# Optimization experiments

Measured on AMD Instinct MI355X. Metric: run time of the kernel, lower is better.

## Reference

```python
import jax, jax.numpy as jnp
import numpy as np
import math

B, T, C = 2, 2048, 1024
H, DK, DV = 16, 64, 64


def setup_inputs() -> dict:
    key = jax.random.key(0)
    ks = jax.random.split(key, 5)
    # randw(*d) = randn(*d) / sqrt(d[-1])
    x = jax.random.normal(ks[0], (B, T, C), dtype=jnp.float32)
    w_q = jax.random.normal(ks[1], (H, DK, C), dtype=jnp.float32) / math.sqrt(C)
    w_k = jax.random.normal(ks[2], (H, DK, C), dtype=jnp.float32) / math.sqrt(C)
    w_v = jax.random.normal(ks[3], (H, DV, C), dtype=jnp.float32) / math.sqrt(C)
    w_o = jax.random.normal(ks[4], (H * DV, C), dtype=jnp.float32) / math.sqrt(C)
    return {"x": x, "w_q": w_q, "w_k": w_k, "w_v": w_v, "w_o": w_o}


def reference(x, w_q, w_k, w_v, w_o):
    # Full prefill: bs_q.first = 0, bs_q.nb = T, causal=True, dropout=0 (eval).
    dk = w_q.shape[1]
    q = jnp.einsum('ntc,hdc->nhtd', x, w_q)  # [B,H,T,DK]
    k = jnp.einsum('ntc,hdc->nhtd', x, w_k)  # [B,H,T,DK]
    v = jnp.einsum('ntc,hdc->nhtd', x, w_v)  # [B,H,T,DV]
    a = jnp.einsum('nhtd,nhsd->nhts', q, k) / jnp.sqrt(jnp.asarray(dk, x.dtype))
    # amm_generator: mask where query_idx < key_idx (strict upper triangle)
    t = a.shape[-1]
    mask = jnp.arange(t)[:, None] < jnp.arange(t)[None, :]  # [T,T] bool
    a = jnp.where(mask[None, None], jnp.asarray(-jnp.inf, a.dtype), a)
    a = jax.nn.softmax(a, axis=-1)
    y = jnp.einsum('nhts,nhsd->nthd', a, v)  # [B,T,H,DV]
    y = y.reshape(y.shape[0], y.shape[1], -1)  # [B,T,H*DV]
    return y @ w_o  # [B,T,C]
```

## Files before the change

kernel.cpp:

```cpp
#include <hip/hip_runtime.h>
#include <hip/hip_bf16.h>

#define B_ 2
#define T_ 2048
#define C_ 1024
#define H_ 16
#define D_ 64

typedef __attribute__((ext_vector_type(8))) short bf16x8;
typedef __attribute__((ext_vector_type(4))) float f32x4;
typedef __attribute__((ext_vector_type(8))) unsigned short u16x8;
typedef __attribute__((ext_vector_type(2))) unsigned int u32x2;
typedef __attribute__((ext_vector_type(4))) unsigned int u32x4;

__device__ __forceinline__ unsigned short bf1(float a) {
    __bf16 x = (__bf16)a;
    return __builtin_bit_cast(unsigned short, x);
}
__device__ __forceinline__ unsigned int pk2(float a, float b) {
    return (unsigned int)bf1(a) | ((unsigned int)bf1(b) << 16);
}

__device__ __forceinline__ void gll16(const void* g, void* l) {
    __builtin_amdgcn_global_load_lds(
        (const __attribute__((address_space(1))) unsigned int*)g,
        (__attribute__((address_space(3))) unsigned int*)l, 16, 0, 0);
}

__global__ __launch_bounds__(256) void prep_x(
    const float* __restrict__ x, unsigned short* __restrict__ xb)
{
    const size_t i = ((size_t)blockIdx.x * 256 + threadIdx.x) * 16;
    float4 f0 = *reinterpret_cast<const float4*>(x + i);
    float4 f1 = *reinterpret_cast<const float4*>(x + i + 4);
    float4 f2 = *reinterpret_cast<const float4*>(x + i + 8);
    float4 f3 = *reinterpret_cast<const float4*>(x + i + 12);
    u32x4 a = {pk2(f0.x, f0.y), pk2(f0.z, f0.w), pk2(f1.x, f1.y), pk2(f1.z, f1.w)};
    u32x4 b = {pk2(f2.x, f2.y), pk2(f2.z, f2.w), pk2(f3.x, f3.y), pk2(f3.z, f3.w)};
    *reinterpret_cast<u32x4*>(xb + i) = a;
    *reinterpret_cast<u32x4*>(xb + i + 8) = b;
}

__global__ __launch_bounds__(256) void prep_w(
    const float* __restrict__ wq, const float* __restrict__ wk,
    const float* __restrict__ wv, unsigned short* __restrict__ wb)
{
    const int bid = blockIdx.x, tid = threadIdx.x;
    const int rb = bid * 4;
    const float* src = (rb < 1024) ? wq + (size_t)rb * 1024
                     : (rb < 2048) ? wk + (size_t)(rb - 1024) * 1024
                                   : wv + (size_t)(rb - 2048) * 1024;
    const float sc = (rb < 1024) ? 0.125f * 1.4426950408889634f : 1.0f;
    const float4* s4 = (const float4*)src;
    u32x2* d = (u32x2*)(wb + (size_t)rb * 1024);
#pragma unroll
    for (int k = 0; k < 4; k++) {
        float4 v = s4[k * 256 + tid];
        u32x2 w;
        w[0] = pk2(v.x * sc, v.y * sc);
        w[1] = pk2(v.z * sc, v.w * sc);
        d[k * 256 + tid] = w;
    }
}

__global__ __launch_bounds__(256) void prep_wo(
    const float* __restrict__ wo, unsigned short* __restrict__ wt)
{
    __shared__ unsigned short tile[64][72];
    const int tk = (blockIdx.x & 15) << 6, tn = (blockIdx.x >> 4) << 6;
    const int r = threadIdx.x >> 2, cb = (threadIdx.x & 3) << 4;
#pragma unroll
    for (int j = 0; j < 4; j++) {
        float4 v = *reinterpret_cast<const float4*>(
            wo + (size_t)(tk + r) * 1024 + tn + cb + j * 4);
        u32x2 w;
        w[0] = pk2(v.x, v.y);
        w[1] = pk2(v.z, v.w);
        *reinterpret_cast<u32x2*>(&tile[r][cb + j * 4]) = w;
    }
    __syncthreads();
    unsigned short buf[16];
#pragma unroll
    for (int j = 0; j < 16; j++) buf[j] = tile[cb + j][r];
    unsigned short* dst = wt + (size_t)(tn + r) * 1024 + tk + cb;
    *reinterpret_cast<u16x8*>(dst) = *reinterpret_cast<u16x8*>(buf);
    *reinterpret_cast<u16x8*>(dst + 8) = *reinterpret_cast<u16x8*>(buf + 8);
}

__global__ __launch_bounds__(256) void qkv_gemm(
    const unsigned short* __restrict__ xb, const unsigned short* __restrict__ wb,
    unsigned short* __restrict__ qkv)
{
    __shared__ __align__(16) unsigned short As[2][128 * 64];
    __shared__ __align__(16) unsigned short Bs[2][128 * 64];
    const int tid = threadIdx.x;
    const int lane = tid & 63, wave = tid >> 6;
    const int g = lane >> 4, c16 = lane & 15;
    const int xcd = blockIdx.x & 7, idx = blockIdx.x >> 3;
    const int bm = (xcd << 2) + idx / 24, bn = idx % 24;
    const int jbase = bn << 7;
    const int which = jbase >> 10;

    const int srow = wave * 32 + (lane >> 3);
    const int swc = ((lane & 7) ^ (lane >> 3)) << 3;
    const unsigned short* asrc = xb + ((size_t)(bm << 7) + srow) * C_ + swc;
    const unsigned short* bsrc = wb + ((size_t)(bn << 7) + srow) * C_ + swc;

    f32x4 acc[4][4];
#pragma unroll
    for (int i = 0; i < 4; i++)
#pragma unroll
        for (int j = 0; j < 4; j++) acc[i][j] = (f32x4){0.f, 0.f, 0.f, 0.f};

    const int wm = (wave >> 1) << 6, wn = (wave & 1) << 6;

    auto stage = [&](int buf, int k0) {
#pragma unroll
        for (int i = 0; i < 4; i++) {
            gll16(asrc + k0 + i * 8 * C_, &As[buf][(wave * 32 + i * 8) << 6]);
            gll16(bsrc + k0 + i * 8 * C_, &Bs[buf][(wave * 32 + i * 8) << 6]);
        }
    };

    stage(0, 0);
    int cur = 0;
    for (int t = 0; t < 16; ++t) {
        __syncthreads();
        if (t < 15) stage(cur ^ 1, (t + 1) << 6);
#pragma unroll
        for (int kk = 0; kk < 2; kk++) {
            bf16x8 af[4], bfv[4];
#pragma unroll
            for (int m = 0; m < 4; m++)
                af[m] = *reinterpret_cast<const bf16x8*>(
                    &As[cur][((wm + m * 16 + c16) << 6) + ((((kk << 2) + g) ^ (c16 & 7)) << 3)]);
#pragma unroll
            for (int n = 0; n < 4; n++)
                bfv[n] = *reinterpret_cast<const bf16x8*>(
                    &Bs[cur][((wn + n * 16 + c16) << 6) + ((((kk << 2) + g) ^ (c16 & 7)) << 3)]);
#pragma unroll
            for (int m = 0; m < 4; m++)
#pragma unroll
                for (int n = 0; n < 4; n++)
                    acc[m][n] = __builtin_amdgcn_mfma_f32_16x16x32_bf16(af[m], bfv[n], acc[m][n], 0, 0, 0);
        }
        cur ^= 1;
    }

#pragma unroll
    for (int m = 0; m < 4; m++) {
        const int grow = (bm << 7) + wm + m * 16 + (g << 2);
#pragma unroll
        for (int n = 0; n < 4; n++) {
            const int j = jbase + wn + n * 16 + c16;
            const int jj = j & 1023;
            const int h = jj >> 6, d = jj & 63;
#pragma unroll
            for (int r = 0; r < 4; r++) {
                const int row = grow + r;
                const int b = row >> 11, t = row & 2047;
                const size_t off = ((size_t)((which * B_ + b) * H_ + h) * T_ + t) * 64 + d;
                qkv[off] = bf1(acc[m][n][r]);
            }
        }
    }
}

__device__ __forceinline__ void attn_tile(
    const unsigned short* __restrict__ Ks, const unsigned short* __restrict__ Vt,
    unsigned short* __restrict__ Psw,
    const bf16x8& qf0, const bf16x8& qf1,
    float& m_run, float& l_run, f32x4* acc,
    int qglob, int s0, bool diag, int g, int c16)
{
    f32x4 sfT[4];
#pragma unroll
    for (int f = 0; f < 4; f++) sfT[f] = (f32x4){0.f, 0.f, 0.f, 0.f};

    __builtin_amdgcn_s_setprio(1);
#pragma unroll
    for (int f = 0; f < 4; f++) {
        const int row = f * 16 + c16;
        const int sw = row & 7;
        bf16x8 k0 = *reinterpret_cast<const bf16x8*>(&Ks[(row << 6) + ((g ^ sw) << 3)]);
        bf16x8 k1 = *reinterpret_cast<const bf16x8*>(&Ks[(row << 6) + (((g + 4) ^ sw) << 3)]);
        sfT[f] = __builtin_amdgcn_mfma_f32_16x16x32_bf16(k0, qf0, sfT[f], 0, 0, 0);
        sfT[f] = __builtin_amdgcn_mfma_f32_16x16x32_bf16(k1, qf1, sfT[f], 0, 0, 0);
    }
    __builtin_amdgcn_s_setprio(0);

    if (diag) {
#pragma unroll
        for (int f = 0; f < 4; f++)
#pragma unroll
            for (int r = 0; r < 4; r++) {
                const int kv = s0 + f * 16 + g * 4 + r;
                if (kv > qglob) sfT[f][r] = -1e30f;
            }
    }

    float mloc = -1e30f;
#pragma unroll
    for (int f = 0; f < 4; f++)
#pragma unroll
        for (int r = 0; r < 4; r++) mloc = fmaxf(mloc, sfT[f][r]);
    mloc = fmaxf(mloc, __shfl_xor(mloc, 16, 64));
    mloc = fmaxf(mloc, __shfl_xor(mloc, 32, 64));
    const float mn = fmaxf(m_run, mloc);
    const float corr = __builtin_amdgcn_exp2f(m_run - mn);
    m_run = mn;
    float ssum = 0.f;
#pragma unroll
    for (int f = 0; f < 4; f++)
#pragma unroll
        for (int r = 0; r < 4; r++) {
            const float pv = __builtin_amdgcn_exp2f(sfT[f][r] - mn);
            sfT[f][r] = pv;
            ssum += pv;
        }
    ssum += __shfl_xor(ssum, 16, 64);
    ssum += __shfl_xor(ssum, 32, 64);
    l_run = l_run * corr + ssum;
#pragma unroll
    for (int fd = 0; fd < 4; fd++)
#pragma unroll
        for (int r = 0; r < 4; r++) acc[fd][r] *= corr;

#pragma unroll
    for (int f = 0; f < 4; f++) {
        u32x2 w;
        w[0] = pk2(sfT[f][0], sfT[f][1]);
        w[1] = pk2(sfT[f][2], sfT[f][3]);
        *reinterpret_cast<u32x2*>(&Psw[c16 * 72 + f * 16 + g * 4]) = w;
    }

    __builtin_amdgcn_s_setprio(1);
#pragma unroll
    for (int ks = 0; ks < 2; ks++) {
        bf16x8 pa = *reinterpret_cast<const bf16x8*>(&Psw[c16 * 72 + ks * 32 + (g << 3)]);
#pragma unroll
        for (int fd = 0; fd < 4; fd++) {
            const int d = fd * 16 + c16;
            bf16x8 vf = *reinterpret_cast<const bf16x8*>(
                &Vt[d * 72 + ((((ks << 2) + g) ^ ((d >> 3) & 7)) << 3)]);
            acc[fd] = __builtin_amdgcn_mfma_f32_16x16x32_bf16(vf, pa, acc[fd], 0, 0, 0);
        }
    }
    __builtin_amdgcn_s_setprio(0);
}

__global__ __launch_bounds__(256) void attn(
    const unsigned short* __restrict__ qkv, unsigned short* __restrict__ y)
{
    __shared__ __align__(16) unsigned short Ks[64 * 64];
    __shared__ __align__(16) unsigned short Vt[64 * 72];
    __shared__ __align__(16) unsigned short Ps[4][16 * 72];
    const int tid = threadIdx.x, lane = tid & 63, wave = tid >> 6;
    const int g = lane >> 4, c16 = lane & 15;
    const int p = blockIdx.x & 15;
    const int bh = blockIdx.x >> 4;
    const int b = bh >> 4, h = bh & 15;
    const size_t headoff = (size_t)(b * H_ + h) * T_ * 64;
    const size_t QSZ = (size_t)B_ * H_ * T_ * 64;
    const unsigned short* qp = qkv + headoff;
    const unsigned short* kp = qkv + QSZ + headoff;
    const unsigned short* vp = qkv + 2 * QSZ + headoff;

    const int tA = p, tB = 31 - p;
    const int qbaseA = (tA << 6) + wave * 16, qbaseB = (tB << 6) + wave * 16;

    bf16x8 qfA[2], qfB[2];
    {
        const size_t ra = (size_t)(qbaseA + c16) * 64, rb = (size_t)(qbaseB + c16) * 64;
        qfA[0] = *reinterpret_cast<const bf16x8*>(qp + ra + g * 8);
        qfA[1] = *reinterpret_cast<const bf16x8*>(qp + ra + 32 + g * 8);
        qfB[0] = *reinterpret_cast<const bf16x8*>(qp + rb + g * 8);
        qfB[1] = *reinterpret_cast<const bf16x8*>(qp + rb + 32 + g * 8);
    }

    float mA = -1e30f, lA = 0.f, mB = -1e30f, lB = 0.f;
    f32x4 accA[4], accB[4];
#pragma unroll
    for (int i = 0; i < 4; i++) {
        accA[i] = (f32x4){0.f, 0.f, 0.f, 0.f};
        accB[i] = (f32x4){0.f, 0.f, 0.f, 0.f};
    }

    const int krow = tid >> 2, kc2 = (tid & 3) << 1;
    const int vr2 = (tid >> 3) << 1, vds = (tid & 7) << 3;

    const int nt = 32 - p;
    for (int it = 0; it < nt; ++it) {
        const int s0 = it << 6;
        __syncthreads();
        {
            const unsigned short* src = kp + (size_t)(s0 + krow) * 64 + (kc2 << 3);
            u16x8 a0 = *reinterpret_cast<const u16x8*>(src);
            u16x8 a1 = *reinterpret_cast<const u16x8*>(src + 8);
            const int sw = krow & 7;
            *reinterpret_cast<u16x8*>(&Ks[(krow << 6) + ((kc2 ^ sw) << 3)]) = a0;
            *reinterpret_cast<u16x8*>(&Ks[(krow << 6) + (((kc2 + 1) ^ sw) << 3)]) = a1;
        }
        {
            const unsigned short* sp = vp + (size_t)(s0 + vr2) * 64 + vds;
            u16x8 v0 = *reinterpret_cast<const u16x8*>(sp);
            u16x8 v1 = *reinterpret_cast<const u16x8*>(sp + 64);
#pragma unroll
            for (int i = 0; i < 8; i++) {
                const int d = vds + i;
                const unsigned int w = (unsigned int)v0[i] | ((unsigned int)v1[i] << 16);
                const int idx = d * 72 + ((((vr2 >> 3) ^ ((d >> 3) & 7)) << 3) | (vr2 & 7));
                *reinterpret_cast<unsigned int*>(&Vt[idx]) = w;
            }
        }
        __syncthreads();

        attn_tile(Ks, Vt, Ps[wave], qfB[0], qfB[1], mB, lB, accB,
                  qbaseB + c16, s0, it == tB, g, c16);
        if (it <= tA)
            attn_tile(Ks, Vt, Ps[wave], qfA[0], qfA[1], mA, lA, accA,
                      qbaseA + c16, s0, it == tA, g, c16);
    }

    const float liA = 1.0f / lA, liB = 1.0f / lB;
#pragma unroll
    for (int fd = 0; fd < 4; fd++) {
        u32x2 wa, wb2;
        wa[0] = pk2(accA[fd][0] * liA, accA[fd][1] * liA);
        wa[1] = pk2(accA[fd][2] * liA, accA[fd][3] * liA);
        wb2[0] = pk2(accB[fd][0] * liB, accB[fd][1] * liB);
        wb2[1] = pk2(accB[fd][2] * liB, accB[fd][3] * liB);
        const size_t ca = ((size_t)b * T_ + qbaseA + c16) * 1024 + h * 64 + fd * 16 + g * 4;
        const size_t cb = ((size_t)b * T_ + qbaseB + c16) * 1024 + h * 64 + fd * 16 + g * 4;
        *reinterpret_cast<u32x2*>(&y[ca]) = wa;
        *reinterpret_cast<u32x2*>(&y[cb]) = wb2;
    }
}

__global__ __launch_bounds__(256) void out_proj(
    const unsigned short* __restrict__ y, const unsigned short* __restrict__ wt,
    float* __restrict__ out)
{
    __shared__ __align__(16) unsigned short As[2][128 * 64];
    __shared__ __align__(16) unsigned short Bs[2][128 * 64];
    const int tid = threadIdx.x;
    const int lane = tid & 63, wave = tid >> 6;
    const int g = lane >> 4, c16 = lane & 15;
    const int xcd = blockIdx.x & 7, idx = blockIdx.x >> 3;
    const int bm = (xcd << 2) + (idx >> 3), bn = idx & 7;
    const int wm = (wave >> 1) << 6, wn = (wave & 1) << 6;

    const int srow = wave * 32 + (lane >> 3);
    const int swc = ((lane & 7) ^ (lane >> 3)) << 3;
    const unsigned short* ysrc = y + ((size_t)(bm << 7) + srow) * 1024 + swc;
    const unsigned short* wsrc = wt + ((size_t)(bn << 7) + srow) * 1024 + swc;

    f32x4 acc[4][4];
#pragma unroll
    for (int i = 0; i < 4; i++)
#pragma unroll
        for (int j = 0; j < 4; j++) acc[i][j] = (f32x4){0.f, 0.f, 0.f, 0.f};

    auto stage = [&](int buf, int k0) {
#pragma unroll
        for (int i = 0; i < 4; i++) {
            gll16(ysrc + k0 + i * 8 * 1024, &As[buf][(wave * 32 + i * 8) << 6]);
            gll16(wsrc + k0 + i * 8 * 1024, &Bs[buf][(wave * 32 + i * 8) << 6]);
        }
    };

    stage(0, 0);
    int cur = 0;
    for (int t = 0; t < 16; ++t) {
        __syncthreads();
        if (t < 15) stage(cur ^ 1, (t + 1) << 6);
#pragma unroll
        for (int kk = 0; kk < 2; kk++) {
            bf16x8 af[4], bfr[4];
#pragma unroll
            for (int m = 0; m < 4; m++)
                af[m] = *reinterpret_cast<const bf16x8*>(
                    &As[cur][((wm + m * 16 + c16) << 6) + ((((kk << 2) + g) ^ (c16 & 7)) << 3)]);
#pragma unroll
            for (int n = 0; n < 4; n++)
                bfr[n] = *reinterpret_cast<const bf16x8*>(
                    &Bs[cur][((wn + n * 16 + c16) << 6) + ((((kk << 2) + g) ^ (c16 & 7)) << 3)]);
#pragma unroll
            for (int m = 0; m < 4; m++)
#pragma unroll
                for (int n = 0; n < 4; n++)
                    acc[m][n] = __builtin_amdgcn_mfma_f32_16x16x32_bf16(af[m], bfr[n], acc[m][n], 0, 0, 0);
        }
        cur ^= 1;
    }

#pragma unroll
    for (int m = 0; m < 4; m++) {
        const int grow = (bm << 7) + wm + m * 16 + (g << 2);
#pragma unroll
        for (int n = 0; n < 4; n++) {
            const int gcol = (bn << 7) + wn + n * 16 + c16;
#pragma unroll
            for (int r = 0; r < 4; r++)
                out[(size_t)(grow + r) * 1024 + gcol] = acc[m][n][r];
        }
    }
}

extern "C" void kernel_launch(void* const* d_in, const int* in_sizes, int n_in,
                              void* d_out, int out_size, void* d_ws, size_t ws_size,
                              hipStream_t stream) {
    const float* x  = (const float*)d_in[0];
    const float* wq = (const float*)d_in[1];
    const float* wk = (const float*)d_in[2];
    const float* wv = (const float*)d_in[3];
    const float* wo = (const float*)d_in[4];
    float* out = (float*)d_out;

    unsigned short* wb  = (unsigned short*)d_ws;
    unsigned short* y   = (unsigned short*)d_ws;
    unsigned short* qkv = (unsigned short*)d_ws + (size_t)4 * 1024 * 1024;
    unsigned short* wt  = qkv;
    unsigned short* xb  = (unsigned short*)d_out;

    prep_x<<<dim3(1024), 256, 0, stream>>>(x, xb);
    prep_w<<<dim3(768), 256, 0, stream>>>(wq, wk, wv, wb);
    qkv_gemm<<<dim3(768), 256, 0, stream>>>(xb, wb, qkv);
    attn<<<dim3(16 * B_ * H_), 256, 0, stream>>>(qkv, y);
    prep_wo<<<dim3(256), 256, 0, stream>>>(wo, wt);
    out_proj<<<dim3(256), 256, 0, stream>>>(y, wt, out);
}
```

Measured before the change: 128.9 us.

## Store V transposed and double-buffer K/V tiles with async global-to-LDS loads

The QKV projection epilogue now writes V in a [d][t] transposed layout using packed 4-element stores. Attention stages K and the pre-transposed V directly into swizzled LDS via global_load_lds, double-buffered, so the next tile's load overlaps the current tile's compute. This removes the per-element register transpose of V and drops one barrier per iteration. The cost is twice the K/V LDS footprint, and correctness depends on the barrier waiting for the async loads to finish.

```diff
diff --git a/kernel.cpp b/kernel.cpp
--- a/kernel.cpp
+++ b/kernel.cpp
@@ -147,20 +147,37 @@
         cur ^= 1;
     }
 
-#pragma unroll
-    for (int m = 0; m < 4; m++) {
-        const int grow = (bm << 7) + wm + m * 16 + (g << 2);
-#pragma unroll
-        for (int n = 0; n < 4; n++) {
-            const int j = jbase + wn + n * 16 + c16;
-            const int jj = j & 1023;
-            const int h = jj >> 6, d = jj & 63;
-#pragma unroll
-            for (int r = 0; r < 4; r++) {
-                const int row = grow + r;
-                const int b = row >> 11, t = row & 2047;
-                const size_t off = ((size_t)((which * B_ + b) * H_ + h) * T_ + t) * 64 + d;
-                qkv[off] = bf1(acc[m][n][r]);
+    if (which < 2) {
+#pragma unroll
+        for (int m = 0; m < 4; m++) {
+            const int grow = (bm << 7) + wm + m * 16 + (g << 2);
+#pragma unroll
+            for (int n = 0; n < 4; n++) {
+                const int jj = (jbase + wn + n * 16 + c16) & 1023;
+                const int h = jj >> 6, d = jj & 63;
+#pragma unroll
+                for (int r = 0; r < 4; r++) {
+                    const int row = grow + r;
+                    const int b = row >> 11, t = row & 2047;
+                    const size_t off = ((size_t)((which * B_ + b) * H_ + h) * T_ + t) * 64 + d;
+                    qkv[off] = bf1(acc[m][n][r]);
+                }
+            }
+        }
+    } else {
+#pragma unroll
+        for (int m = 0; m < 4; m++) {
+            const int grow = (bm << 7) + wm + m * 16 + (g << 2);
+            const int b = grow >> 11, t = grow & 2047;
+#pragma unroll
+            for (int n = 0; n < 4; n++) {
+                const int jj = (jbase + wn + n * 16 + c16) & 1023;
+                const int h = jj >> 6, d = jj & 63;
+                u32x2 w;
+                w[0] = pk2(acc[m][n][0], acc[m][n][1]);
+                w[1] = pk2(acc[m][n][2], acc[m][n][3]);
+                const size_t off = ((size_t)((2 * B_ + b) * H_ + h) * 64 + d) * T_ + t;
+                *reinterpret_cast<u32x2*>(&qkv[off]) = w;
             }
         }
     }
@@ -242,7 +259,7 @@
         for (int fd = 0; fd < 4; fd++) {
             const int d = fd * 16 + c16;
             bf16x8 vf = *reinterpret_cast<const bf16x8*>(
-                &Vt[d * 72 + ((((ks << 2) + g) ^ ((d >> 3) & 7)) << 3)]);
+                &Vt[(d << 6) + ((((ks << 2) + g) ^ (d & 7)) << 3)]);
             acc[fd] = __builtin_amdgcn_mfma_f32_16x16x32_bf16(vf, pa, acc[fd], 0, 0, 0);
         }
     }
@@ -252,8 +269,8 @@
 __global__ __launch_bounds__(256) void attn(
     const unsigned short* __restrict__ qkv, unsigned short* __restrict__ y)
 {
-    __shared__ __align__(16) unsigned short Ks[64 * 64];
-    __shared__ __align__(16) unsigned short Vt[64 * 72];
+    __shared__ __align__(16) unsigned short Ks[2][64 * 64];
+    __shared__ __align__(16) unsigned short Vt[2][64 * 64];
     __shared__ __align__(16) unsigned short Ps[4][16 * 72];
     const int tid = threadIdx.x, lane = tid & 63, wave = tid >> 6;
     const int g = lane >> 4, c16 = lane & 15;
@@ -264,7 +281,7 @@
     const size_t QSZ = (size_t)B_ * H_ * T_ * 64;
     const unsigned short* qp = qkv + headoff;
     const unsigned short* kp = qkv + QSZ + headoff;
-    const unsigned short* vp = qkv + 2 * QSZ + headoff;
+    const unsigned short* vTp = qkv + 2 * QSZ + headoff;
 
     const int tA = p, tB = 31 - p;
     const int qbaseA = (tA << 6) + wave * 16, qbaseB = (tB << 6) + wave * 16;
@@ -286,40 +303,33 @@
         accB[i] = (f32x4){0.f, 0.f, 0.f, 0.f};
     }
 
-    const int krow = tid >> 2, kc2 = (tid & 3) << 1;
-    const int vr2 = (tid >> 3) << 1, vds = (tid & 7) << 3;
+    const int srow8 = lane >> 3;
+    const int swc = ((lane & 7) ^ srow8) << 3;
+    const unsigned short* ksrc = kp + (size_t)(wave * 16 + srow8) * 64 + swc;
+    const unsigned short* vsrc = vTp + (size_t)(wave * 16 + srow8) * T_ + swc;
+
+    auto stage = [&](int buf, int s0) {
+#pragma unroll
+        for (int i = 0; i < 2; i++) {
+            gll16(ksrc + (size_t)(s0 + i * 8) * 64, &Ks[buf][(wave * 16 + i * 8) << 6]);
+            gll16(vsrc + s0 + (size_t)i * 8 * T_, &Vt[buf][(wave * 16 + i * 8) << 6]);
+        }
+    };
 
     const int nt = 32 - p;
+    stage(0, 0);
+    int cur = 0;
     for (int it = 0; it < nt; ++it) {
+        __syncthreads();
+        if (it + 1 < nt) stage(cur ^ 1, (it + 1) << 6);
         const int s0 = it << 6;
-        __syncthreads();
-        {
-            const unsigned short* src = kp + (size_t)(s0 + krow) * 64 + (kc2 << 3);
-            u16x8 a0 = *reinterpret_cast<const u16x8*>(src);
-            u16x8 a1 = *reinterpret_cast<const u16x8*>(src + 8);
-            const int sw = krow & 7;
-            *reinterpret_cast<u16x8*>(&Ks[(krow << 6) + ((kc2 ^ sw) << 3)]) = a0;
-            *reinterpret_cast<u16x8*>(&Ks[(krow << 6) + (((kc2 + 1) ^ sw) << 3)]) = a1;
-        }
-        {
-            const unsigned short* sp = vp + (size_t)(s0 + vr2) * 64 + vds;
-            u16x8 v0 = *reinterpret_cast<const u16x8*>(sp);
-            u16x8 v1 = *reinterpret_cast<const u16x8*>(sp + 64);
-#pragma unroll
-            for (int i = 0; i < 8; i++) {
-                const int d = vds + i;
-                const unsigned int w = (unsigned int)v0[i] | ((unsigned int)v1[i] << 16);
-                const int idx = d * 72 + ((((vr2 >> 3) ^ ((d >> 3) & 7)) << 3) | (vr2 & 7));
-                *reinterpret_cast<unsigned int*>(&Vt[idx]) = w;
-            }
-        }
-        __syncthreads();
-
-        attn_tile(Ks, Vt, Ps[wave], qfB[0], qfB[1], mB, lB, accB,
+
+        attn_tile(Ks[cur], Vt[cur], Ps[wave], qfB[0], qfB[1], mB, lB, accB,
                   qbaseB + c16, s0, it == tB, g, c16);
         if (it <= tA)
-            attn_tile(Ks, Vt, Ps[wave], qfA[0], qfA[1], mA, lA, accA,
+            attn_tile(Ks[cur], Vt[cur], Ps[wave], qfA[0], qfA[1], mA, lA, accA,
                       qbaseA + c16, s0, it == tA, g, c16);
+        cur ^= 1;
     }
 
     const float liA = 1.0f / lA, liB = 1.0f / lB;
```

Result: no change. 129.9 us (+0.7%).
